# Kernel optimization log

Measured on AMD Instinct MI355X. Metric: run time of the kernel, lower is better.

## Reference

```python
import jax, jax.numpy as jnp
import numpy as np
import math

T, N, P, H, E, S, R = 64, 1024, 256, 256, 512, 16, 16

def _sincos(n, d):
    pos = np.arange(n)[:, None].astype(np.float32)
    div = np.exp(np.arange(0, d, 2).astype(np.float32) * -(math.log(10000.0) / d))
    pe = np.zeros((n, d), np.float32)
    pe[:, 0::2] = np.sin(pos * div)
    pe[:, 1::2] = np.cos(pos * div)
    return jnp.asarray(pe)

def setup_inputs():
    key = jax.random.key(0)
    ks = iter(jax.random.split(key, 40))
    def w(shape, s=0.05):
        return jax.random.normal(next(ks), shape, jnp.float32) * s
    adj_seq = (jax.random.uniform(next(ks), (T, N, N)) < 0.05).astype(jnp.float32)
    return dict(
        adj_seq=adj_seq,
        pos_emb=_sincos(N, P),
        g1_Wm=w((P, H)), g1_bm=jnp.zeros((H,), jnp.float32),
        g1_Wq=w((H, H)), g1_Wk=w((H, H)), g1_gb=jnp.asarray(-1.0, jnp.float32),
        g1_Wu=w((P + H, H)), g1_bu=jnp.zeros((H,), jnp.float32),
        g1_lg=jnp.ones((H,), jnp.float32), g1_lb=jnp.zeros((H,), jnp.float32),
        g2_Wm=w((H, H)), g2_bm=jnp.zeros((H,), jnp.float32),
        g2_Wu=w((2 * H, H)), g2_bu=jnp.zeros((H,), jnp.float32),
        g2_lg=jnp.ones((H,), jnp.float32), g2_lb=jnp.zeros((H,), jnp.float32),
        m_lg=jnp.ones((H,), jnp.float32), m_lb=jnp.zeros((H,), jnp.float32),
        m_Win=w((H, 2 * E)), m_bin=jnp.zeros((2 * E,), jnp.float32),
        m_Wdelta=w((E, R)), m_bdelta=jnp.zeros((R,), jnp.float32),
        m_Wdt=w((R, E)), m_bdt=jnp.zeros((E,), jnp.float32),
        m_WB=w((E, S)), m_bB=jnp.zeros((S,), jnp.float32),
        m_WC=w((E, S)), m_bC=jnp.zeros((S,), jnp.float32),
        m_Alog=-jnp.exp(w((E, S), 0.1)),
        m_D=jnp.zeros((E,), jnp.float32),
        m_Wout=w((E, H)), m_bout=jnp.zeros((H,), jnp.float32),
    )

def _ln(x, g, b):
    mu = x.mean(-1, keepdims=True)
    v = ((x - mu) ** 2).mean(-1, keepdims=True)
    return (x - mu) / jnp.sqrt(v + 1e-5) * g + b

def reference(adj_seq, pos_emb, g1_Wm, g1_bm, g1_Wq, g1_Wk, g1_gb, g1_Wu, g1_bu,
              g1_lg, g1_lb, g2_Wm, g2_bm, g2_Wu, g2_bu, g2_lg, g2_lb,
              m_lg, m_lb, m_Win, m_bin, m_Wdelta, m_bdelta, m_Wdt, m_bdt,
              m_WB, m_bB, m_WC, m_bC, m_Alog, m_D, m_Wout, m_bout):
    scale = math.sqrt(H) * max(1.0, 1e-6)  # sqrt(d) * gate_temperature

    def encode(adj):  # adj: [N,N]
        msgs = pos_emb @ g1_Wm + g1_bm                 # [N,H]
        q = msgs @ g1_Wq
        k = msgs @ g1_Wk
        gates = jax.nn.sigmoid(q @ k.T / scale + g1_gb)
        agg = (gates * adj) @ msgs                     # gated aggregation
        x = _ln(jax.nn.relu(jnp.concatenate([pos_emb, agg], -1) @ g1_Wu + g1_bu), g1_lg, g1_lb)
        msgs2 = x @ g2_Wm + g2_bm
        agg2 = adj @ msgs2                             # ungated layer 2
        x = _ln(jax.nn.relu(jnp.concatenate([x, agg2], -1) @ g2_Wu + g2_bu), g2_lg, g2_lb)
        return x                                       # [N,H]

    seq = jax.vmap(encode)(adj_seq)                    # [T,N,H]
    x = seq.transpose(1, 0, 2)                         # [N,T,H] node-batched sequences

    # --- MambaBlock ---
    res = x
    xn = _ln(x, m_lg, m_lb)
    xp = xn @ m_Win + m_bin
    u, gate = jnp.split(xp, 2, axis=-1)                # [N,T,E] each
    u = jax.nn.silu(u)
    delta = jax.nn.softplus((u @ m_Wdelta + m_bdelta) @ m_Wdt + m_bdt)  # [N,T,E]
    Bm = u @ m_WB + m_bB                               # [N,T,S]
    Cm = u @ m_WC + m_bC                               # [N,T,S]
    A = -jnp.exp(m_Alog)                               # [E,S]

    def step(h, inp):
        u_t, d_t, B_t, C_t = inp                       # [N,E],[N,E],[N,S],[N,S]
        Ad = jnp.exp(d_t[:, :, None] * A[None])        # [N,E,S]
        h = Ad * h + d_t[:, :, None] * B_t[:, None, :] * u_t[:, :, None]
        y = jnp.einsum('ns,nes->ne', C_t, h)
        return h, y

    h0 = jnp.zeros((N, E, S), x.dtype)
    _, ys = jax.lax.scan(step, h0, (u.transpose(1, 0, 2), delta.transpose(1, 0, 2),
                                    Bm.transpose(1, 0, 2), Cm.transpose(1, 0, 2)))
    y = ys.transpose(1, 0, 2)                          # [N,T,E]
    y = (y + u * m_D) * jax.nn.silu(gate)
    out = y @ m_Wout + m_bout + res                    # [N,T,H]
    return out.transpose(1, 0, 2)                      # [T,N,H]
```

## Files before the change

### kernel.cpp

```cpp
#include <hip/hip_runtime.h>
#include <hip/hip_bf16.h>

typedef __hip_bfloat16 bf16;
typedef __attribute__((ext_vector_type(8))) short s16x8;
typedef __attribute__((ext_vector_type(4))) short s16x4;
typedef __attribute__((ext_vector_type(4))) float f32x4;

#define TT 64
#define NN_ 1024
#define EE 512

__device__ __forceinline__ float toF(float v) { return v; }
__device__ __forceinline__ float toF(bf16 v) { return __bfloat162float(v); }
__device__ __forceinline__ bf16 f2b(float v) { return __float2bfloat16(v); }

#if __has_builtin(__builtin_amdgcn_exp2f)
#define EXP2F(x) __builtin_amdgcn_exp2f(x)
#else
#define EXP2F(x) exp2f(x)
#endif
#if __has_builtin(__builtin_amdgcn_logf)
#define LOG2F(x) __builtin_amdgcn_logf(x)
#else
#define LOG2F(x) log2f(x)
#endif

enum { EPI_F32 = 0, EPI_SIG_F32 = 1, EPI_SIG_B16 = 2 };
enum { E_LN1 = 0, E_BF16 = 1, E_LN2 = 2, E_SILU = 3, E_OUT = 4, E_TRI = 5, E_BF16T = 6 };

template <bool TRANSB, int EPI>
__global__ __launch_bounds__(256) void gemm_k(
    const float* __restrict__ A, const float* __restrict__ B,
    float* __restrict__ outF, const float* __restrict__ bias,
    const float* __restrict__ sbeta, float alpha,
    int M, int Nn, int K, int lda, int ldb)
{
    __shared__ float As[16][68];
    __shared__ float Bs[16][68];
    const int tid = threadIdx.x;
    const int tx = tid & 15, ty = tid >> 4;
    const int m0 = blockIdx.x * 64, n0 = blockIdx.y * 64;
    float acc[4][4] = {};

    for (int k0 = 0; k0 < K; k0 += 16) {
        {
            int row = tid >> 2, kk0 = (tid & 3) * 4, grow = m0 + row;
#pragma unroll
            for (int j = 0; j < 4; j++) {
                int kk = kk0 + j, gk = k0 + kk;
                As[kk][row] = (grow < M) ? A[(size_t)grow * lda + gk] : 0.f;
            }
        }
        if (!TRANSB) {
            int kk = tid >> 4, c0 = (tid & 15) * 4;
#pragma unroll
            for (int j = 0; j < 4; j++) {
                int col = c0 + j, gn = n0 + col;
                Bs[kk][col] = (gn < Nn) ? B[(size_t)(k0 + kk) * ldb + gn] : 0.f;
            }
        } else {
            int col = tid >> 2, kk0 = (tid & 3) * 4, gn = n0 + col;
#pragma unroll
            for (int j = 0; j < 4; j++) {
                int kk = kk0 + j;
                Bs[kk][col] = (gn < Nn) ? B[(size_t)gn * ldb + (k0 + kk)] : 0.f;
            }
        }
        __syncthreads();
#pragma unroll
        for (int kk = 0; kk < 16; kk++) {
            float a[4], b[4];
#pragma unroll
            for (int i = 0; i < 4; i++) a[i] = As[kk][ty * 4 + i];
#pragma unroll
            for (int j = 0; j < 4; j++) b[j] = Bs[kk][tx * 4 + j];
#pragma unroll
            for (int i = 0; i < 4; i++)
#pragma unroll
                for (int j = 0; j < 4; j++)
                    acc[i][j] = fmaf(a[i], b[j], acc[i][j]);
        }
        __syncthreads();
    }

    float gb = (EPI != EPI_F32 && sbeta) ? sbeta[0] : 0.f;
#pragma unroll
    for (int i = 0; i < 4; i++) {
        int row = m0 + ty * 4 + i;
        if (row >= M) continue;
#pragma unroll
        for (int j = 0; j < 4; j++) {
            int col = n0 + tx * 4 + j;
            if (col >= Nn) continue;
            float v = acc[i][j];
            if (EPI == EPI_F32) {
                if (bias) v += bias[col];
                outF[(size_t)row * Nn + col] = v;
            } else if (EPI == EPI_SIG_F32) {
                v = v * alpha + gb;
                outF[(size_t)row * Nn + col] = 1.f / (1.f + __expf(-v));
            } else {
                v = v * alpha + gb;
                ((bf16*)outF)[(size_t)row * Nn + col] = f2b(1.f / (1.f + __expf(-v)));
            }
        }
    }
}

template <int BM, int BN, bool CAT, int EPI>
__global__ __launch_bounds__(256) void mfma_k(
    const bf16* __restrict__ A1, const bf16* __restrict__ A2, unsigned rowmask,
    const bf16* __restrict__ BT, const float* __restrict__ bias,
    float* __restrict__ outF,
    bf16* __restrict__ outB, bf16* __restrict__ outB2,
    const float* __restrict__ g1, const float* __restrict__ b1,
    const float* __restrict__ g2, const float* __restrict__ b2,
    const bf16* __restrict__ resid,
    int M, int K)
{
    constexpr bool LN = (EPI == E_LN1 || EPI == E_LN2);
    constexpr int STAGE_B = (BM * 32 + BN * 32) * 2;
    constexpr int SB = LN ? (64 * 260 * 4) : STAGE_B;
    __shared__ __align__(16) char smem[SB];
    short* As = (short*)smem;
    short* Bs = As + BM * 32;
    float* Cs = (float*)smem;

    const int tid = threadIdx.x;
    const int wid = tid >> 6, lane = tid & 63;
    const int wr = (BN == 256) ? 0 : wid;
    const int wc = (BN == 256) ? wid : 0;
    const int m0 = blockIdx.x * BM, n0 = blockIdx.y * BN;
    const int srow = tid >> 2;
    const int skoff = (tid & 3) * 8;

    f32x4 acc[4][4] = {};
    s16x8 pa[BM / 64], pbv[BN / 64];

    auto LOADT = [&](int k0) {
#pragma unroll
        for (int c = 0; c < BM / 64; c++) {
            int r = c * 64 + srow;
            int gr = m0 + r;
            const bf16* p;
            if (CAT) {
                int gk = k0 + skoff;
                p = (gk < 256) ? (A1 + (size_t)(gr & rowmask) * 256 + gk)
                               : (A2 + (size_t)gr * 256 + (gk - 256));
            } else {
                p = A1 + (size_t)gr * K + k0 + skoff;
            }
            pa[c] = *(const s16x8*)p;
        }
#pragma unroll
        for (int c = 0; c < BN / 64; c++) {
            int r = c * 64 + srow;
            pbv[c] = *(const s16x8*)(BT + (size_t)(n0 + r) * K + k0 + skoff);
        }
    };

    LOADT(0);
#pragma unroll 1
    for (int k0 = 0; k0 < K; k0 += 32) {
#pragma unroll
        for (int c = 0; c < BM / 64; c++)
            *(s16x8*)&As[(c * 64 + srow) * 32 + skoff] = pa[c];
#pragma unroll
        for (int c = 0; c < BN / 64; c++)
            *(s16x8*)&Bs[(c * 64 + srow) * 32 + skoff] = pbv[c];
        __syncthreads();
        if (k0 + 32 < K) LOADT(k0 + 32);
        s16x8 af[4], bf[4];
#pragma unroll
        for (int mi = 0; mi < 4; mi++)
            af[mi] = *(s16x8*)&As[(wr * 64 + mi * 16 + (lane & 15)) * 32 + (lane >> 4) * 8];
#pragma unroll
        for (int ni = 0; ni < 4; ni++)
            bf[ni] = *(s16x8*)&Bs[(wc * 64 + ni * 16 + (lane & 15)) * 32 + (lane >> 4) * 8];
#pragma unroll
        for (int mi = 0; mi < 4; mi++)
#pragma unroll
            for (int ni = 0; ni < 4; ni++)
                acc[mi][ni] = __builtin_amdgcn_mfma_f32_16x16x32_bf16(
                    af[mi], bf[ni], acc[mi][ni], 0, 0, 0);
        __syncthreads();
    }

    if (EPI == E_TRI) {
#pragma unroll
        for (int mi = 0; mi < 4; mi++)
#pragma unroll
            for (int ni = 0; ni < 4; ni++)
#pragma unroll
                for (int r = 0; r < 4; r++) {
                    int row = m0 + wid * 64 + mi * 16 + (lane >> 4) * 4 + r;
                    int col = ni * 16 + (lane & 15);
                    if (col < 48) {
                        float v = acc[mi][ni][r] + bias[col];
                        outF[(size_t)row * 48 + col] = v;
                    }
                }
    } else {
#pragma unroll
        for (int mi = 0; mi < 4; mi++)
#pragma unroll
            for (int ni = 0; ni < 4; ni++)
#pragma unroll
                for (int r = 0; r < 4; r++) {
                    int rl = mi * 16 + (lane >> 4) * 4 + r;
                    int cl = wc * 64 + ni * 16 + (lane & 15);
                    Cs[rl * 260 + cl] = fmaxf(acc[mi][ni][r] + bias[cl], 0.f);
                }
        __syncthreads();
        float g1v[4], b1v[4], g2v[4], b2v[4];
#pragma unroll
        for (int i = 0; i < 4; i++) {
            g1v[i] = g1[lane * 4 + i];
            b1v[i] = b1[lane * 4 + i];
            if (EPI == E_LN2) { g2v[i] = g2[lane * 4 + i]; b2v[i] = b2[lane * 4 + i]; }
        }
        for (int rr = 0; rr < 16; rr++) {
            int rl = wid * 16 + rr;
            int grow = m0 + rl;
            float x[4];
#pragma unroll
            for (int i = 0; i < 4; i++) x[i] = Cs[rl * 260 + lane * 4 + i];
            float s = x[0] + x[1] + x[2] + x[3];
#pragma unroll
            for (int o = 1; o < 64; o <<= 1) s += __shfl_xor(s, o, 64);
            float mu = s * (1.f / 256.f);
            float d[4], ss = 0.f;
#pragma unroll
            for (int i = 0; i < 4; i++) { d[i] = x[i] - mu; ss = fmaf(d[i], d[i], ss); }
#pragma unroll
            for (int o = 1; o < 64; o <<= 1) ss += __shfl_xor(ss, o, 64);
            float inv = rsqrtf(fmaxf(ss * (1.f / 256.f), 0.f) + 1e-5f);
            float y[4];
#pragma unroll
            for (int i = 0; i < 4; i++) y[i] = d[i] * inv * g1v[i] + b1v[i];
            if (EPI == E_LN1) {
                __align__(8) bf16 pk[4];
#pragma unroll
                for (int i = 0; i < 4; i++) pk[i] = f2b(y[i]);
                *(s16x4*)&outB[(size_t)grow * 256 + lane * 4] = *(s16x4*)pk;
            } else {
                int trow = (grow & 1023) * 64 + (grow >> 10);
                __align__(8) bf16 pk[4];
#pragma unroll
                for (int i = 0; i < 4; i++) pk[i] = f2b(y[i]);
                *(s16x4*)&outB[(size_t)trow * 256 + lane * 4] = *(s16x4*)pk;
                float s2 = y[0] + y[1] + y[2] + y[3];
#pragma unroll
                for (int o = 1; o < 64; o <<= 1) s2 += __shfl_xor(s2, o, 64);
                float mu2 = s2 * (1.f / 256.f);
                float d2[4], ss2 = 0.f;
#pragma unroll
                for (int i = 0; i < 4; i++) { d2[i] = y[i] - mu2; ss2 = fmaf(d2[i], d2[i], ss2); }
#pragma unroll
                for (int o = 1; o < 64; o <<= 1) ss2 += __shfl_xor(ss2, o, 64);
                float inv2 = rsqrtf(fmaxf(ss2 * (1.f / 256.f), 0.f) + 1e-5f);
                __align__(8) bf16 pk2[4];
#pragma unroll
                for (int i = 0; i < 4; i++) pk2[i] = f2b(d2[i] * inv2 * g2v[i] + b2v[i]);
                *(s16x4*)&outB2[(size_t)trow * 256 + lane * 4] = *(s16x4*)pk2;
            }
        }
    }
}

template <int EPI>
__global__ __launch_bounds__(256, 2) void mfma2_k(
    const bf16* __restrict__ A, const bf16* __restrict__ BT,
    const float* __restrict__ bias,
    float* __restrict__ outF, bf16* __restrict__ outB, bf16* __restrict__ outB2,
    const bf16* __restrict__ resid,
    int K)
{
    constexpr int STAGE_B = (128 * 40 + 256 * 40) * 2;
    constexpr int TRB = (EPI == E_BF16T) ? (64 * 268 * 2) : 0;
    constexpr int SB = STAGE_B > TRB ? STAGE_B : TRB;
    __shared__ __align__(16) char smem[SB];
    short* As = (short*)smem;
    short* Bs = As + 128 * 40;

    const int tid = threadIdx.x;
    const int wid = tid >> 6, lane = tid & 63;
    const int wr = wid & 1;
    const int wc = wid >> 1;
    const int m0 = blockIdx.x * 128, n0 = blockIdx.y * 256;
    const int srow = tid >> 2;
    const int skoff = (tid & 3) * 8;

    f32x4 acc[4][8] = {};
    s16x8 pa[2], pb[4];

    auto LOADT = [&](int k0) {
#pragma unroll
        for (int c = 0; c < 2; c++)
            pa[c] = *(const s16x8*)(A + (size_t)(m0 + c * 64 + srow) * K + k0 + skoff);
#pragma unroll
        for (int c = 0; c < 4; c++)
            pb[c] = *(const s16x8*)(BT + (size_t)(n0 + c * 64 + srow) * K + k0 + skoff);
    };

    LOADT(0);
#pragma unroll 1
    for (int k0 = 0; k0 < K; k0 += 32) {
#pragma unroll
        for (int c = 0; c < 2; c++)
            *(s16x8*)&As[(c * 64 + srow) * 40 + skoff] = pa[c];
#pragma unroll
        for (int c = 0; c < 4; c++)
            *(s16x8*)&Bs[(c * 64 + srow) * 40 + skoff] = pb[c];
        __syncthreads();
        if (k0 + 32 < K) LOADT(k0 + 32);
        s16x8 af[4];
#pragma unroll
        for (int mi = 0; mi < 4; mi++)
            af[mi] = *(s16x8*)&As[(wr * 64 + mi * 16 + (lane & 15)) * 40 + (lane >> 4) * 8];
#pragma unroll
        for (int ni = 0; ni < 8; ni++) {
            s16x8 bfv = *(s16x8*)&Bs[(wc * 128 + ni * 16 + (lane & 15)) * 40 + (lane >> 4) * 8];
#pragma unroll
            for (int mi = 0; mi < 4; mi++)
                acc[mi][ni] = __builtin_amdgcn_mfma_f32_16x16x32_bf16(
                    af[mi], bfv, acc[mi][ni], 0, 0, 0);
        }
        __syncthreads();
    }

    if (EPI == E_SILU) {
#pragma unroll
        for (int mi = 0; mi < 4; mi++)
#pragma unroll
            for (int ni = 0; ni < 8; ni++)
#pragma unroll
                for (int r = 0; r < 4; r++) {
                    int row = m0 + wr * 64 + mi * 16 + (lane >> 4) * 4 + r;
                    int col = n0 + wc * 128 + ni * 16 + (lane & 15);
                    float v = acc[mi][ni][r] + bias[col];
                    float s = v / (1.f + __expf(-v));
                    if (col < EE) outB[(size_t)row * EE + col] = f2b(s);
                    else          outB2[(size_t)row * EE + (col - EE)] = f2b(s);
                }
    } else if (EPI == E_OUT) {
#pragma unroll
        for (int mi = 0; mi < 4; mi++)
#pragma unroll
            for (int ni = 0; ni < 8; ni++)
#pragma unroll
                for (int r = 0; r < 4; r++) {
                    int row = m0 + wr * 64 + mi * 16 + (lane >> 4) * 4 + r;
                    int col = n0 + wc * 128 + ni * 16 + (lane & 15);
                    float v = acc[mi][ni][r] + bias[col] + toF(resid[(size_t)row * 256 + col]);
                    int t = row & 63, n = row >> 6;
                    outF[((size_t)t * NN_ + n) * 256 + col] = v;
                }
    } else {
        short* Ts = (short*)smem;
#pragma unroll 1
        for (int h = 0; h < 2; h++) {
            if (h) __syncthreads();
            if (wr == h) {
#pragma unroll
                for (int mi = 0; mi < 4; mi++)
#pragma unroll
                    for (int ni = 0; ni < 8; ni++)
#pragma unroll
                        for (int r = 0; r < 4; r++) {
                            int rl = mi * 16 + (lane >> 4) * 4 + r;
                            int cl = wc * 128 + ni * 16 + (lane & 15);
                            union { bf16 b; short s; } u;
                            u.b = f2b(acc[mi][ni][r] + bias[n0 + cl]);
                            Ts[rl * 268 + cl] = u.s;
                        }
            }
            __syncthreads();
            const int col = tid;
            const int rowbase = m0 + h * 64;
            size_t dbase = (((size_t)(rowbase >> 10)) * 256 + (n0 + col)) * 1024 + (rowbase & 1023);
#pragma unroll
            for (int j0 = 0; j0 < 64; j0 += 8) {
                s16x8 v;
#pragma unroll
                for (int i = 0; i < 8; i++) v[i] = Ts[(j0 + i) * 268 + col];
                *(s16x8*)&outB[dbase + j0] = v;
            }
        }
    }
}

__global__ __launch_bounds__(256) void packadj_k(
    const float4* __restrict__ adj4, unsigned int* __restrict__ bits32)
{
    const size_t nwords = (size_t)TT * NN_ * NN_ / 32;
    const size_t stride = (size_t)gridDim.x * 256;
    for (size_t w = (size_t)blockIdx.x * 256 + threadIdx.x; w < nwords; w += stride) {
        const float4* __restrict__ p = adj4 + w * 8;
        float4 v[8];
#pragma unroll
        for (int i = 0; i < 8; i++) v[i] = p[i];
        unsigned int m = 0;
#pragma unroll
        for (int i = 0; i < 8; i++) {
            m |= (v[i].x != 0.f ? 1u : 0u) << (4 * i);
            m |= (v[i].y != 0.f ? 2u : 0u) << (4 * i);
            m |= (v[i].z != 0.f ? 4u : 0u) << (4 * i);
            m |= (v[i].w != 0.f ? 8u : 0u) << (4 * i);
        }
        bits32[w] = m;
    }
}

template <bool GATED>
__global__ __launch_bounds__(256, 2) void aggmm_k(
    const unsigned char* __restrict__ adjbits, const bf16* __restrict__ gatesb,
    const bf16* __restrict__ BTsrc, bf16* __restrict__ out)
{
    __shared__ __align__(16) short As[128 * 40];
    __shared__ __align__(16) short Bs[256 * 40];
    const int tid = threadIdx.x;
    const int wid = tid >> 6, lane = tid & 63;
    const int wr = wid & 1;
    const int wc = wid >> 1;
    const int bx = blockIdx.x;
    const int t = bx >> 3, n0 = (bx & 7) * 128;
    const int srow = tid >> 2;
    const int skoff = (tid & 3) * 8;

    const unsigned char* __restrict__ abB =
        adjbits + ((size_t)t * 1024 + n0) * 128 + (tid & 3);
    const bf16* __restrict__ gB = GATED ? (gatesb + (size_t)n0 * 1024 + skoff) : nullptr;
    const bf16* __restrict__ bt = GATED ? BTsrc : (BTsrc + (size_t)t * 256 * 1024);
    const size_t orow0 = (size_t)t * 1024 + n0;

    f32x4 acc[4][8] = {};

    unsigned char pm[2];
    s16x8 pg[2];
    s16x8 pb[4];

    auto LOADA = [&](int k0) {
#pragma unroll
        for (int c = 0; c < 2; c++) {
            int r = c * 64 + srow;
            pm[c] = abB[(size_t)r * 128 + (k0 >> 3)];
            if (GATED) pg[c] = *(const s16x8*)(gB + (size_t)r * 1024 + k0);
        }
#pragma unroll
        for (int c = 0; c < 4; c++)
            pb[c] = *(const s16x8*)(bt + (size_t)(c * 64 + srow) * 1024 + k0 + skoff);
    };
    auto STORE = [&]() {
#pragma unroll
        for (int c = 0; c < 2; c++) {
            unsigned m = pm[c];
            s16x8 tmp;
            if (GATED) {
#pragma unroll
                for (int i = 0; i < 8; i++) tmp[i] = ((m >> i) & 1) ? pg[c][i] : (short)0;
            } else {
#pragma unroll
                for (int i = 0; i < 8; i++) tmp[i] = ((m >> i) & 1) ? (short)0x3F80 : (short)0;
            }
            *(s16x8*)&As[(c * 64 + srow) * 40 + skoff] = tmp;
        }
#pragma unroll
        for (int c = 0; c < 4; c++)
            *(s16x8*)&Bs[(c * 64 + srow) * 40 + skoff] = pb[c];
    };

    LOADA(0);
#pragma unroll 1
    for (int k0 = 0; k0 < 1024; k0 += 32) {
        STORE();
        __syncthreads();
        if (k0 + 32 < 1024) LOADA(k0 + 32);
        s16x8 af[4];
#pragma unroll
        for (int mi = 0; mi < 4; mi++)
            af[mi] = *(s16x8*)&As[(wr * 64 + mi * 16 + (lane & 15)) * 40 + (lane >> 4) * 8];
#pragma unroll
        for (int ni = 0; ni < 8; ni++) {
            s16x8 bfv = *(s16x8*)&Bs[(wc * 128 + ni * 16 + (lane & 15)) * 40 + (lane >> 4) * 8];
#pragma unroll
            for (int mi = 0; mi < 4; mi++)
                acc[mi][ni] = __builtin_amdgcn_mfma_f32_16x16x32_bf16(
                    af[mi], bfv, acc[mi][ni], 0, 0, 0);
        }
        __syncthreads();
    }

#pragma unroll
    for (int mi = 0; mi < 4; mi++)
#pragma unroll
        for (int ni = 0; ni < 8; ni++)
#pragma unroll
            for (int r = 0; r < 4; r++) {
                int rowl = wr * 64 + mi * 16 + (lane >> 4) * 4 + r;
                int col = wc * 128 + ni * 16 + (lane & 15);
                out[(orow0 + rowl) * 256 + col] = f2b(acc[mi][ni][r]);
            }
}

__global__ __launch_bounds__(256) void scan_k(
    const bf16* __restrict__ u, const bf16* __restrict__ sg,
    const float* __restrict__ dbc,
    const float* __restrict__ Wdt, const float* __restrict__ bdt,
    const float* __restrict__ Alog, const float* __restrict__ D,
    bf16* __restrict__ yg)
{
    const int n = blockIdx.x, e = blockIdx.y * 256 + threadIdx.x;
    float al[16], wdt[16], h[16];
#pragma unroll
    for (int s = 0; s < 16; s++) {
        al[s] = -__expf(Alog[e * 16 + s]) * 1.44269504f;
        h[s] = 0.f;
    }
#pragma unroll
    for (int k = 0; k < 16; k++) wdt[k] = Wdt[(size_t)k * EE + e];
    const float bdte = bdt[e], De = D[e];
    const float* __restrict__ rowp = dbc + (size_t)n * TT * 48;
    const size_t base = (size_t)n * TT * EE + e;
#pragma unroll 2
    for (int t = 0; t < TT; t++) {
        const float* __restrict__ r = rowp + t * 48;
        float a0 = bdte, a1 = 0.f, a2 = 0.f, a3 = 0.f;
#pragma unroll
        for (int k = 0; k < 4; k++) {
            a0 = fmaf(r[k],      wdt[k],      a0);
            a1 = fmaf(r[k + 4],  wdt[k + 4],  a1);
            a2 = fmaf(r[k + 8],  wdt[k + 8],  a2);
            a3 = fmaf(r[k + 12], wdt[k + 12], a3);
        }
        float acc = (a0 + a1) + (a2 + a3);
        float delta = (acc > 20.f)
            ? acc
            : 0.69314718056f * LOG2F(1.f + EXP2F(acc * 1.44269504f));
        size_t idx = base + (size_t)t * EE;
        float uv = toF(u[idx]);
        float du = delta * uv;
        float y0 = 0.f, y1 = 0.f, y2 = 0.f, y3 = 0.f;
#pragma unroll
        for (int s = 0; s < 16; s += 4) {
            float ad0 = EXP2F(delta * al[s]);
            float ad1 = EXP2F(delta * al[s + 1]);
            float ad2 = EXP2F(delta * al[s + 2]);
            float ad3 = EXP2F(delta * al[s + 3]);
            h[s]     = fmaf(ad0, h[s],     du * r[16 + s]);
            h[s + 1] = fmaf(ad1, h[s + 1], du * r[17 + s]);
            h[s + 2] = fmaf(ad2, h[s + 2], du * r[18 + s]);
            h[s + 3] = fmaf(ad3, h[s + 3], du * r[19 + s]);
            y0 = fmaf(r[32 + s], h[s],     y0);
            y1 = fmaf(r[33 + s], h[s + 1], y1);
            y2 = fmaf(r[34 + s], h[s + 2], y2);
            y3 = fmaf(r[35 + s], h[s + 3], y3);
        }
        float y = (y0 + y1) + (y2 + y3);
        yg[idx] = f2b((y + uv * De) * toF(sg[idx]));
    }
}

__global__ void cast_k(const float* __restrict__ in, bf16* __restrict__ out, int n) {
    int i = blockIdx.x * 256 + threadIdx.x;
    if (i < n) out[i] = f2b(in[i]);
}
__global__ void transT_k(const float* __restrict__ W, bf16* __restrict__ out, int K, int Nn) {
    int gid = blockIdx.x * 256 + threadIdx.x;
    if (gid >= K * Nn) return;
    int n = gid / K, k = gid - n * K;
    out[gid] = f2b(W[(size_t)k * Nn + n]);
}
__global__ void transmsgs_k(const float* __restrict__ msgs, bf16* __restrict__ msgsT) {
    int gid = blockIdx.x * 256 + threadIdx.x;
    int c = gid >> 10, j = gid & 1023;
    msgsT[gid] = f2b(msgs[(size_t)j * 256 + c]);
}
__global__ void wdbct_k(const float* __restrict__ Wd, const float* __restrict__ WB,
                        const float* __restrict__ WC, bf16* __restrict__ out,
                        const float* __restrict__ bd, const float* __restrict__ bB,
                        const float* __restrict__ bC, float* __restrict__ biascat) {
    int gid = blockIdx.x * 256 + threadIdx.x;
    if (gid < 48) biascat[gid] = (gid < 16) ? bd[gid] : (gid < 32) ? bB[gid - 16] : bC[gid - 32];
    if (gid >= 64 * 512) return;
    int n = gid >> 9, k = gid & 511;
    float v = 0.f;
    if (n < 16)      v = Wd[(size_t)k * 16 + n];
    else if (n < 32) v = WB[(size_t)k * 16 + (n - 16)];
    else if (n < 48) v = WC[(size_t)k * 16 + (n - 32)];
    out[gid] = f2b(v);
}

extern "C" void kernel_launch(void* const* d_in, const int* in_sizes, int n_in,
                              void* d_out, int out_size, void* d_ws, size_t ws_size,
                              hipStream_t stream)
{
    const float* adj   = (const float*)d_in[0];
    const float* pos   = (const float*)d_in[1];
    const float* g1Wm  = (const float*)d_in[2];
    const float* g1bm  = (const float*)d_in[3];
    const float* g1Wq  = (const float*)d_in[4];
    const float* g1Wk  = (const float*)d_in[5];
    const float* g1gb  = (const float*)d_in[6];
    const float* g1Wu  = (const float*)d_in[7];
    const float* g1bu  = (const float*)d_in[8];
    const float* g1lg  = (const float*)d_in[9];
    const float* g1lb  = (const float*)d_in[10];
    const float* g2Wm  = (const float*)d_in[11];
    const float* g2bm  = (const float*)d_in[12];
    const float* g2Wu  = (const float*)d_in[13];
    const float* g2bu  = (const float*)d_in[14];
    const float* g2lg  = (const float*)d_in[15];
    const float* g2lb  = (const float*)d_in[16];
    const float* mlg   = (const float*)d_in[17];
    const float* mlb   = (const float*)d_in[18];
    const float* mWin  = (const float*)d_in[19];
    const float* mbin  = (const float*)d_in[20];
    const float* mWd   = (const float*)d_in[21];
    const float* mbd   = (const float*)d_in[22];
    const float* mWdt  = (const float*)d_in[23];
    const float* mbdt  = (const float*)d_in[24];
    const float* mWB   = (const float*)d_in[25];
    const float* mbB   = (const float*)d_in[26];
    const float* mWC   = (const float*)d_in[27];
    const float* mbC   = (const float*)d_in[28];
    const float* mAlog = (const float*)d_in[29];
    const float* mD    = (const float*)d_in[30];
    const float* mWout = (const float*)d_in[31];
    const float* mbout = (const float*)d_in[32];
    float* out = (float*)d_out;
    char* ws = (char*)d_ws;

    const size_t BIGE = (size_t)TT * NN_ * 256;
    size_t o = 0;
    auto alloc = [&](size_t bytes) { size_t r = o; o += (bytes + 255) & ~(size_t)255; return r; };

    float* msgs  = (float*)(ws + alloc((size_t)NN_ * 256 * 4));
    float* q     = (float*)(ws + alloc((size_t)NN_ * 256 * 4));
    float* kk    = (float*)(ws + alloc((size_t)NN_ * 256 * 4));
    bf16*  gatesb = (bf16*)(ws + alloc((size_t)NN_ * NN_ * 2));
    unsigned long long* adjbits =
        (unsigned long long*)(ws + alloc((size_t)TT * NN_ * NN_ / 8));
    bf16*  Ra    = (bf16*)(ws + alloc(BIGE * 2));
    size_t off_x1 = alloc(BIGE * 2);
    bf16*  x1    = (bf16*)(ws + off_x1);
    bf16*  agg2  = (bf16*)(ws + alloc(BIGE * 2));
    bf16*  x2    = (bf16*)(ws + alloc(BIGE * 2));
    bf16*  yg    = (bf16*)(ws + alloc(BIGE * 2));
    bf16*  sg    = (bf16*)(ws + alloc((size_t)NN_ * TT * EE * 2));
    float* dbc   = (float*)(ws + alloc((size_t)TT * NN_ * 48 * 4));
    bf16*  u     = (bf16*)(ws + off_x1);
    bf16* posb   = (bf16*)(ws + alloc((size_t)NN_ * 256 * 2));
    bf16* g1WuT  = (bf16*)(ws + alloc((size_t)256 * 512 * 2));
    bf16* g2WmT  = (bf16*)(ws + alloc((size_t)256 * 256 * 2));
    bf16* g2WuT  = (bf16*)(ws + alloc((size_t)256 * 512 * 2));
    bf16* mWinT  = (bf16*)(ws + alloc((size_t)1024 * 256 * 2));
    bf16* mWoutT = (bf16*)(ws + alloc((size_t)256 * 512 * 2));
    bf16* WdBCT  = (bf16*)(ws + alloc((size_t)64 * 512 * 2));
    float* biascat = (float*)(ws + alloc(64 * 4));
    bf16* msgsT  = (bf16*)(ws + alloc((size_t)256 * 1024 * 2));
    bf16* msgs2T = (bf16*)(ws + alloc(BIGE * 2));

    const unsigned ALLR = 0xFFFFFFFFu;
    const int M = TT * NN_;

    packadj_k<<<2048, 256, 0, stream>>>((const float4*)adj, (unsigned int*)adjbits);
    cast_k<<<NN_, 256, 0, stream>>>(pos, posb, NN_ * 256);
    transT_k<<<(512 * 256 + 255) / 256, 256, 0, stream>>>(g1Wu, g1WuT, 512, 256);
    transT_k<<<(256 * 256 + 255) / 256, 256, 0, stream>>>(g2Wm, g2WmT, 256, 256);
    transT_k<<<(512 * 256 + 255) / 256, 256, 0, stream>>>(g2Wu, g2WuT, 512, 256);
    transT_k<<<(256 * 1024 + 255) / 256, 256, 0, stream>>>(mWin, mWinT, 256, 1024);
    transT_k<<<(512 * 256 + 255) / 256, 256, 0, stream>>>(mWout, mWoutT, 512, 256);
    wdbct_k<<<(64 * 512 + 255) / 256, 256, 0, stream>>>(mWd, mWB, mWC, WdBCT, mbd, mbB, mbC, biascat);

    gemm_k<false, EPI_F32><<<dim3(16, 4), 256, 0, stream>>>(
        pos, g1Wm, msgs, g1bm, nullptr, 1.f, NN_, 256, 256, 256, 256);
    transmsgs_k<<<1024, 256, 0, stream>>>(msgs, msgsT);
    gemm_k<false, EPI_F32><<<dim3(16, 4), 256, 0, stream>>>(
        msgs, g1Wq, q, nullptr, nullptr, 1.f, NN_, 256, 256, 256, 256);
    gemm_k<false, EPI_F32><<<dim3(16, 4), 256, 0, stream>>>(
        msgs, g1Wk, kk, nullptr, nullptr, 1.f, NN_, 256, 256, 256, 256);
    gemm_k<true, EPI_SIG_B16><<<dim3(16, 16), 256, 0, stream>>>(
        q, kk, (float*)gatesb, nullptr, g1gb, 1.f / 16.f, NN_, NN_, 256, 256, 256);
    aggmm_k<true><<<512, 256, 0, stream>>>(
        (const unsigned char*)adjbits, gatesb, msgsT, Ra);
    mfma_k<64, 256, true, E_LN1><<<dim3(1024, 1), 256, 0, stream>>>(
        posb, Ra, 1023u, g1WuT, g1bu, nullptr, x1, nullptr,
        g1lg, g1lb, nullptr, nullptr, nullptr, M, 512);
    mfma2_k<E_BF16T><<<dim3(512, 1), 256, 0, stream>>>(
        x1, g2WmT, g2bm, nullptr, msgs2T, nullptr, nullptr, 256);
    aggmm_k<false><<<512, 256, 0, stream>>>(
        (const unsigned char*)adjbits, nullptr, msgs2T, agg2);
    mfma_k<64, 256, true, E_LN2><<<dim3(1024, 1), 256, 0, stream>>>(
        x1, agg2, ALLR, g2WuT, g2bu, nullptr, x2, Ra,
        g2lg, g2lb, mlg, mlb, nullptr, M, 512);
    mfma2_k<E_SILU><<<dim3(512, 4), 256, 0, stream>>>(
        Ra, mWinT, mbin, nullptr, u, sg, nullptr, 256);
    mfma_k<256, 64, false, E_TRI><<<dim3(256, 1), 256, 0, stream>>>(
        u, u, ALLR, WdBCT, biascat, dbc, nullptr, nullptr,
        nullptr, nullptr, nullptr, nullptr, nullptr, M, 512);
    scan_k<<<dim3(NN_, 2), 256, 0, stream>>>(u, sg, dbc, mWdt, mbdt, mAlog, mD, yg);
    mfma2_k<E_OUT><<<dim3(512, 1), 256, 0, stream>>>(
        yg, mWoutT, mbout, out, nullptr, nullptr, x2, 512);

    (void)in_sizes; (void)n_in; (void)out_size; (void)ws_size;
}
```

Before: 1.066 ms.

## Merge prep kernels, fuse Q/K GEMMs, and scan two nodes per thread

Seven weight cast/transpose launches become one grid-stride prep kernel, and the Q and K projection GEMMs become one launch that picks the weight by blockIdx.y. The selective scan now gives each thread two nodes, for more independent work per thread and half as many blocks. This cuts launch overhead and aims to hide scan latency, at the cost of more registers in the scan and lower scan occupancy.

```diff
diff --git a/kernel.cpp b/kernel.cpp
--- a/kernel.cpp
+++ b/kernel.cpp
@@ -107,6 +107,63 @@
     }
 }
 
+__global__ __launch_bounds__(256) void gemmqk_k(
+    const float* __restrict__ A, const float* __restrict__ Bq,
+    const float* __restrict__ Bk, float* __restrict__ outq, float* __restrict__ outk)
+{
+    __shared__ float As[16][68];
+    __shared__ float Bs[16][68];
+    const float* __restrict__ B = (blockIdx.y < 4) ? Bq : Bk;
+    float* __restrict__ outF = (blockIdx.y < 4) ? outq : outk;
+    const int tid = threadIdx.x;
+    const int tx = tid & 15, ty = tid >> 4;
+    const int m0 = blockIdx.x * 64, n0 = (blockIdx.y & 3) * 64;
+    float acc[4][4] = {};
+
+    for (int k0 = 0; k0 < 256; k0 += 16) {
+        {
+            int row = tid >> 2, kk0 = (tid & 3) * 4, grow = m0 + row;
+#pragma unroll
+            for (int j = 0; j < 4; j++) {
+                int kk = kk0 + j;
+                As[kk][row] = A[(size_t)grow * 256 + k0 + kk];
+            }
+        }
+        {
+            int kk = tid >> 4, c0 = (tid & 15) * 4;
+#pragma unroll
+            for (int j = 0; j < 4; j++) {
+                int col = c0 + j;
+                Bs[kk][col] = B[(size_t)(k0 + kk) * 256 + n0 + col];
+            }
+        }
+        __syncthreads();
+#pragma unroll
+        for (int kk = 0; kk < 16; kk++) {
+            float a[4], b[4];
+#pragma unroll
+            for (int i = 0; i < 4; i++) a[i] = As[kk][ty * 4 + i];
+#pragma unroll
+            for (int j = 0; j < 4; j++) b[j] = Bs[kk][tx * 4 + j];
+#pragma unroll
+            for (int i = 0; i < 4; i++)
+#pragma unroll
+                for (int j = 0; j < 4; j++)
+                    acc[i][j] = fmaf(a[i], b[j], acc[i][j]);
+        }
+        __syncthreads();
+    }
+#pragma unroll
+    for (int i = 0; i < 4; i++) {
+        int row = m0 + ty * 4 + i;
+#pragma unroll
+        for (int j = 0; j < 4; j++) {
+            int col = n0 + tx * 4 + j;
+            outF[(size_t)row * 256 + col] = acc[i][j];
+        }
+    }
+}
+
 template <int BM, int BN, bool CAT, int EPI>
 __global__ __launch_bounds__(256) void mfma_k(
     const bf16* __restrict__ A1, const bf16* __restrict__ A2, unsigned rowmask,
@@ -510,85 +567,108 @@
     const float* __restrict__ Alog, const float* __restrict__ D,
     bf16* __restrict__ yg)
 {
-    const int n = blockIdx.x, e = blockIdx.y * 256 + threadIdx.x;
-    float al[16], wdt[16], h[16];
+    const int n0 = blockIdx.x * 2, e = blockIdx.y * 256 + threadIdx.x;
+    float al[16], wdt[16], h0[16], h1[16];
 #pragma unroll
     for (int s = 0; s < 16; s++) {
         al[s] = -__expf(Alog[e * 16 + s]) * 1.44269504f;
-        h[s] = 0.f;
+        h0[s] = 0.f; h1[s] = 0.f;
     }
 #pragma unroll
     for (int k = 0; k < 16; k++) wdt[k] = Wdt[(size_t)k * EE + e];
     const float bdte = bdt[e], De = D[e];
-    const float* __restrict__ rowp = dbc + (size_t)n * TT * 48;
-    const size_t base = (size_t)n * TT * EE + e;
-#pragma unroll 2
+    const float* __restrict__ r0p = dbc + (size_t)n0 * TT * 48;
+    const float* __restrict__ r1p = r0p + TT * 48;
+    const size_t base0 = (size_t)n0 * TT * EE + e;
+    const size_t base1 = base0 + (size_t)TT * EE;
+#pragma unroll 1
     for (int t = 0; t < TT; t++) {
-        const float* __restrict__ r = rowp + t * 48;
-        float a0 = bdte, a1 = 0.f, a2 = 0.f, a3 = 0.f;
-#pragma unroll
-        for (int k = 0; k < 4; k++) {
-            a0 = fmaf(r[k],      wdt[k],      a0);
-            a1 = fmaf(r[k + 4],  wdt[k + 4],  a1);
-            a2 = fmaf(r[k + 8],  wdt[k + 8],  a2);
-            a3 = fmaf(r[k + 12], wdt[k + 12], a3);
-        }
-        float acc = (a0 + a1) + (a2 + a3);
-        float delta = (acc > 20.f)
-            ? acc
-            : 0.69314718056f * LOG2F(1.f + EXP2F(acc * 1.44269504f));
-        size_t idx = base + (size_t)t * EE;
-        float uv = toF(u[idx]);
-        float du = delta * uv;
-        float y0 = 0.f, y1 = 0.f, y2 = 0.f, y3 = 0.f;
-#pragma unroll
-        for (int s = 0; s < 16; s += 4) {
-            float ad0 = EXP2F(delta * al[s]);
-            float ad1 = EXP2F(delta * al[s + 1]);
-            float ad2 = EXP2F(delta * al[s + 2]);
-            float ad3 = EXP2F(delta * al[s + 3]);
-            h[s]     = fmaf(ad0, h[s],     du * r[16 + s]);
-            h[s + 1] = fmaf(ad1, h[s + 1], du * r[17 + s]);
-            h[s + 2] = fmaf(ad2, h[s + 2], du * r[18 + s]);
-            h[s + 3] = fmaf(ad3, h[s + 3], du * r[19 + s]);
-            y0 = fmaf(r[32 + s], h[s],     y0);
-            y1 = fmaf(r[33 + s], h[s + 1], y1);
-            y2 = fmaf(r[34 + s], h[s + 2], y2);
-            y3 = fmaf(r[35 + s], h[s + 3], y3);
-        }
-        float y = (y0 + y1) + (y2 + y3);
-        yg[idx] = f2b((y + uv * De) * toF(sg[idx]));
-    }
-}
-
-__global__ void cast_k(const float* __restrict__ in, bf16* __restrict__ out, int n) {
-    int i = blockIdx.x * 256 + threadIdx.x;
-    if (i < n) out[i] = f2b(in[i]);
-}
-__global__ void transT_k(const float* __restrict__ W, bf16* __restrict__ out, int K, int Nn) {
-    int gid = blockIdx.x * 256 + threadIdx.x;
-    if (gid >= K * Nn) return;
-    int n = gid / K, k = gid - n * K;
-    out[gid] = f2b(W[(size_t)k * Nn + n]);
-}
+        const float* __restrict__ r0 = r0p + t * 48;
+        const float* __restrict__ r1 = r1p + t * 48;
+        float a00 = bdte, a01 = 0.f, a10 = bdte, a11 = 0.f;
+#pragma unroll
+        for (int k = 0; k < 8; k++) {
+            a00 = fmaf(r0[k],     wdt[k],     a00);
+            a01 = fmaf(r0[k + 8], wdt[k + 8], a01);
+            a10 = fmaf(r1[k],     wdt[k],     a10);
+            a11 = fmaf(r1[k + 8], wdt[k + 8], a11);
+        }
+        float acc0 = a00 + a01, acc1 = a10 + a11;
+        float delta0 = (acc0 > 20.f)
+            ? acc0 : 0.69314718056f * LOG2F(1.f + EXP2F(acc0 * 1.44269504f));
+        float delta1 = (acc1 > 20.f)
+            ? acc1 : 0.69314718056f * LOG2F(1.f + EXP2F(acc1 * 1.44269504f));
+        size_t idx0 = base0 + (size_t)t * EE;
+        size_t idx1 = base1 + (size_t)t * EE;
+        float uv0 = toF(u[idx0]), uv1 = toF(u[idx1]);
+        float du0 = delta0 * uv0, du1 = delta1 * uv1;
+        float y00 = 0.f, y01 = 0.f, y10 = 0.f, y11 = 0.f;
+#pragma unroll
+        for (int s = 0; s < 16; s += 2) {
+            float ad00 = EXP2F(delta0 * al[s]);
+            float ad01 = EXP2F(delta0 * al[s + 1]);
+            float ad10 = EXP2F(delta1 * al[s]);
+            float ad11 = EXP2F(delta1 * al[s + 1]);
+            h0[s]     = fmaf(ad00, h0[s],     du0 * r0[16 + s]);
+            h0[s + 1] = fmaf(ad01, h0[s + 1], du0 * r0[17 + s]);
+            h1[s]     = fmaf(ad10, h1[s],     du1 * r1[16 + s]);
+            h1[s + 1] = fmaf(ad11, h1[s + 1], du1 * r1[17 + s]);
+            y00 = fmaf(r0[32 + s], h0[s],     y00);
+            y01 = fmaf(r0[33 + s], h0[s + 1], y01);
+            y10 = fmaf(r1[32 + s], h1[s],     y10);
+            y11 = fmaf(r1[33 + s], h1[s + 1], y11);
+        }
+        float y0 = y00 + y01, y1 = y10 + y11;
+        yg[idx0] = f2b((y0 + uv0 * De) * toF(sg[idx0]));
+        yg[idx1] = f2b((y1 + uv1 * De) * toF(sg[idx1]));
+    }
+}
+
+__global__ __launch_bounds__(256) void prep_all_k(
+    const float* __restrict__ pos,
+    const float* __restrict__ g1Wu, const float* __restrict__ g2Wm,
+    const float* __restrict__ g2Wu, const float* __restrict__ mWin,
+    const float* __restrict__ mWout,
+    const float* __restrict__ Wd, const float* __restrict__ WB,
+    const float* __restrict__ WC, const float* __restrict__ bd,
+    const float* __restrict__ bB, const float* __restrict__ bC,
+    bf16* __restrict__ posb, bf16* __restrict__ g1WuT, bf16* __restrict__ g2WmT,
+    bf16* __restrict__ g2WuT, bf16* __restrict__ mWinT, bf16* __restrict__ mWoutT,
+    bf16* __restrict__ WdBCT, float* __restrict__ biascat)
+{
+    const int total = 262144 + 131072 + 65536 + 131072 + 262144 + 131072 + 32768 + 48;
+    for (int gid = blockIdx.x * 256 + threadIdx.x; gid < total; gid += gridDim.x * 256) {
+        int g = gid;
+        if (g < 262144) { posb[g] = f2b(pos[g]); continue; }
+        g -= 262144;
+        if (g < 131072) { int n = g >> 9, k = g & 511; g1WuT[g] = f2b(g1Wu[(size_t)k * 256 + n]); continue; }
+        g -= 131072;
+        if (g < 65536)  { int n = g >> 8, k = g & 255; g2WmT[g] = f2b(g2Wm[(size_t)k * 256 + n]); continue; }
+        g -= 65536;
+        if (g < 131072) { int n = g >> 9, k = g & 511; g2WuT[g] = f2b(g2Wu[(size_t)k * 256 + n]); continue; }
+        g -= 131072;
+        if (g < 262144) { int n = g >> 8, k = g & 255; mWinT[g] = f2b(mWin[(size_t)k * 1024 + n]); continue; }
+        g -= 262144;
+        if (g < 131072) { int n = g >> 9, k = g & 511; mWoutT[g] = f2b(mWout[(size_t)k * 256 + n]); continue; }
+        g -= 131072;
+        if (g < 32768) {
+            int n = g >> 9, k = g & 511;
+            float v = 0.f;
+            if (n < 16)      v = Wd[(size_t)k * 16 + n];
+            else if (n < 32) v = WB[(size_t)k * 16 + (n - 16)];
+            else if (n < 48) v = WC[(size_t)k * 16 + (n - 32)];
+            WdBCT[g] = f2b(v);
+            continue;
+        }
+        g -= 32768;
+        biascat[g] = (g < 16) ? bd[g] : (g < 32) ? bB[g - 16] : bC[g - 32];
+    }
+}
+
 __global__ void transmsgs_k(const float* __restrict__ msgs, bf16* __restrict__ msgsT) {
     int gid = blockIdx.x * 256 + threadIdx.x;
     int c = gid >> 10, j = gid & 1023;
     msgsT[gid] = f2b(msgs[(size_t)j * 256 + c]);
-}
-__global__ void wdbct_k(const float* __restrict__ Wd, const float* __restrict__ WB,
-                        const float* __restrict__ WC, bf16* __restrict__ out,
-                        const float* __restrict__ bd, const float* __restrict__ bB,
-                        const float* __restrict__ bC, float* __restrict__ biascat) {
-    int gid = blockIdx.x * 256 + threadIdx.x;
-    if (gid < 48) biascat[gid] = (gid < 16) ? bd[gid] : (gid < 32) ? bB[gid - 16] : bC[gid - 32];
-    if (gid >= 64 * 512) return;
-    int n = gid >> 9, k = gid & 511;
-    float v = 0.f;
-    if (n < 16)      v = Wd[(size_t)k * 16 + n];
-    else if (n < 32) v = WB[(size_t)k * 16 + (n - 16)];
-    else if (n < 48) v = WC[(size_t)k * 16 + (n - 32)];
-    out[gid] = f2b(v);
 }
 
 extern "C" void kernel_launch(void* const* d_in, const int* in_sizes, int n_in,
@@ -665,21 +745,14 @@
     const int M = TT * NN_;
 
     packadj_k<<<2048, 256, 0, stream>>>((const float4*)adj, (unsigned int*)adjbits);
-    cast_k<<<NN_, 256, 0, stream>>>(pos, posb, NN_ * 256);
-    transT_k<<<(512 * 256 + 255) / 256, 256, 0, stream>>>(g1Wu, g1WuT, 512, 256);
-    transT_k<<<(256 * 256 + 255) / 256, 256, 0, stream>>>(g2Wm, g2WmT, 256, 256);
-    transT_k<<<(512 * 256 + 255) / 256, 256, 0, stream>>>(g2Wu, g2WuT, 512, 256);
-    transT_k<<<(256 * 1024 + 255) / 256, 256, 0, stream>>>(mWin, mWinT, 256, 1024);
-    transT_k<<<(512 * 256 + 255) / 256, 256, 0, stream>>>(mWout, mWoutT, 512, 256);
-    wdbct_k<<<(64 * 512 + 255) / 256, 256, 0, stream>>>(mWd, mWB, mWC, WdBCT, mbd, mbB, mbC, biascat);
+    prep_all_k<<<1024, 256, 0, stream>>>(
+        pos, g1Wu, g2Wm, g2Wu, mWin, mWout, mWd, mWB, mWC, mbd, mbB, mbC,
+        posb, g1WuT, g2WmT, g2WuT, mWinT, mWoutT, WdBCT, biascat);
 
     gemm_k<false, EPI_F32><<<dim3(16, 4), 256, 0, stream>>>(
         pos, g1Wm, msgs, g1bm, nullptr, 1.f, NN_, 256, 256, 256, 256);
     transmsgs_k<<<1024, 256, 0, stream>>>(msgs, msgsT);
-    gemm_k<false, EPI_F32><<<dim3(16, 4), 256, 0, stream>>>(
-        msgs, g1Wq, q, nullptr, nullptr, 1.f, NN_, 256, 256, 256, 256);
-    gemm_k<false, EPI_F32><<<dim3(16, 4), 256, 0, stream>>>(
-        msgs, g1Wk, kk, nullptr, nullptr, 1.f, NN_, 256, 256, 256, 256);
+    gemmqk_k<<<dim3(16, 8), 256, 0, stream>>>(msgs, g1Wq, g1Wk, q, kk);
     gemm_k<true, EPI_SIG_B16><<<dim3(16, 16), 256, 0, stream>>>(
         q, kk, (float*)gatesb, nullptr, g1gb, 1.f / 16.f, NN_, NN_, 256, 256, 256);
     aggmm_k<true><<<512, 256, 0, stream>>>(
@@ -699,7 +772,7 @@
     mfma_k<256, 64, false, E_TRI><<<dim3(256, 1), 256, 0, stream>>>(
         u, u, ALLR, WdBCT, biascat, dbc, nullptr, nullptr,
         nullptr, nullptr, nullptr, nullptr, nullptr, M, 512);
-    scan_k<<<dim3(NN_, 2), 256, 0, stream>>>(u, sg, dbc, mWdt, mbdt, mAlog, mD, yg);
+    scan_k<<<dim3(NN_ / 2, 2), 256, 0, stream>>>(u, sg, dbc, mWdt, mbdt, mAlog, mD, yg);
     mfma2_k<E_OUT><<<dim3(512, 1), 256, 0, stream>>>(
         yg, mWoutT, mbout, out, nullptr, nullptr, x2, 512);
 
```

Result: faster. 1.030 ms (-3.4%).
